# Performance work log

Measured on AMD Instinct MI355X. Metric: run time of the kernel, lower is better.

Reference implementation:

```python
import jax, jax.numpy as jnp
import numpy as np

FEATURE_DIM = 128

def setup_inputs() -> dict:
    key0 = jax.random.key(0)
    k1, k2, k3 = jax.random.split(key0, 3)
    B, NQ, NK, D = 4, 4096, 4096, FEATURE_DIM
    return {
        "target": jax.random.normal(k1, (B, NQ, D), dtype=jnp.float32),
        "key": jax.random.normal(k2, (B, NK, D), dtype=jnp.float32),
        "value": jax.random.normal(k3, (B, NK, D), dtype=jnp.float32),
    }

def reference(target, key, value):
    # Lan_K F: scores = target @ key^T / sqrt(d); weights = softmax(scores); out = weights @ value
    scale = 1.0 / np.sqrt(FEATURE_DIM).astype(np.float32)
    scores = jnp.einsum('bqd,bkd->bqk', target, key) * scale  # [B, NQ, NK]
    weights = jax.nn.softmax(scores, axis=-1)
    return jnp.einsum('bqk,bkd->bqd', weights, value)  # [B, NQ, D]
```

## Files before the change

kernel.cpp:

```cpp
#include <hip/hip_runtime.h>
#include <stdint.h>

#define B_ 4
#define NQ_ 4096
#define NK_ 4096
#define D_ 128
#define BM_ 32
#define BN_ 128
#define NITER_ (NK_/BN_)
#define PS_ 136
#define OS_ 66

typedef __attribute__((ext_vector_type(8))) short short8;
typedef __attribute__((ext_vector_type(4))) float floatx4;
typedef unsigned int u32;

union frag_u { u32 u[4]; short8 s; };
union pair_u { u32 u[2]; uint2 v; };

__device__ __forceinline__ unsigned short f2bf_rne(float x){
  union { float f; u32 u; } c; c.f = x;
  u32 u = c.u;
  return (unsigned short)((u + 0x7fffu + ((u >> 16) & 1u)) >> 16);
}
__device__ __forceinline__ u32 pk2bf(float a, float b){
  union { float f; u32 u; } x, y; x.f = a; y.f = b;
  return ((x.u + 0x8000u) >> 16) | ((y.u + 0x8000u) & 0xffff0000u);
}

__global__ __launch_bounds__(256) void prep_kernel(
    const float* __restrict__ k, const float* __restrict__ v,
    unsigned short* __restrict__ kf, unsigned short* __restrict__ vf){
  __shared__ __align__(16) char smem[40960];
  const int t = threadIdx.x;
  const int blk = blockIdx.x;
  if (blk < 128){
    int b = blk >> 5, it = blk & 31;
    const float* src = k + ((size_t)b*NK_ + it*BN_)*D_;
    #pragma unroll
    for (int i = 0; i < 16; i++){
      int f = t + i*256;
      int row = f >> 5, c4 = f & 31;
      float4 a = *(const float4*)(src + (size_t)row*D_ + c4*4);
      ushort4 s;
      s.x = f2bf_rne(a.x); s.y = f2bf_rne(a.y);
      s.z = f2bf_rne(a.z); s.w = f2bf_rne(a.w);
      int kg = row >> 5, rem = row & 31;
      int dh = (rem >> 2) & 1;
      int l15 = ((rem >> 3) << 2) | (rem & 3);
      int wq = kg*2 + dh;
      int j = c4 >> 3, l4 = (c4 >> 1) & 3, half = c4 & 1;
      *(ushort4*)(smem + (wq*4 + j)*1088 + l4*272 + l15*16 + half*8) = s;
    }
    __syncthreads();
    unsigned short* dst = kf + (size_t)(b*32 + it)*2048*8;
    #pragma unroll
    for (int i = 0; i < 8; i++){
      int c = t + i*256;
      int lane = c & 63, j = (c >> 6) & 3, wq = c >> 8;
      int l15 = lane & 15, l4 = lane >> 4;
      short8 x = *(const short8*)(smem + (wq*4 + j)*1088 + l4*272 + l15*16);
      *(short8*)(dst + (size_t)c*8) = x;
    }
  } else {
    int blk2 = blk - 128;
    int b = blk2 >> 5, it = blk2 & 31;
    const float* src = v + ((size_t)b*NK_ + it*BN_)*D_;
    #pragma unroll
    for (int i = 0; i < 16; i++){
      int f = t + i*256;
      int row = f >> 5, c4 = f & 31;
      float4 a = *(const float4*)(src + (size_t)row*D_ + c4*4);
      float vals[4] = {a.x, a.y, a.z, a.w};
      int kk = row & 7, l4a = (row >> 3) & 3, kga = row >> 5;
      #pragma unroll
      for (int jj = 0; jj < 4; jj++){
        int d = c4*4 + jj;
        int dh = d >> 6, dt = (d >> 4) & 3, l15 = d & 15;
        int c = ((kga*2 + dh)*4 + dt)*64 + l4a*16 + l15;
        *(unsigned short*)(smem + c*16 + (c>>2)*16 + kk*2) = f2bf_rne(vals[jj]);
      }
    }
    __syncthreads();
    unsigned short* dst = vf + (size_t)(b*32 + it)*2048*8;
    #pragma unroll
    for (int i = 0; i < 8; i++){
      int c = t + i*256;
      short8 x = *(const short8*)(smem + c*16 + (c>>2)*16);
      *(short8*)(dst + (size_t)c*8) = x;
    }
  }
}

__global__ __launch_bounds__(512, 4) void attn_kernel(
    const float* __restrict__ Qf, const unsigned short* __restrict__ Kb,
    const unsigned short* __restrict__ Vt, float* __restrict__ Out){
  __shared__ __align__(16) char sm[34816];
  unsigned short* smP = (unsigned short*)sm;
  float* smO = (float*)sm;
  float* smL = (float*)(sm + 33792);

  const int bi = blockIdx.x;
  const int b  = (bi >> 1) & 3;
  const int qt = ((bi >> 3) << 1) | (bi & 1);
  const int q0 = qt * BM_;
  const int tid = threadIdx.x;
  const int w = tid >> 6, lane = tid & 63;
  const int kg = w >> 1, dh = w & 1;
  const int l15 = lane & 15, l4 = lane >> 4;

  const short8* Kfrag = (const short8*)Kb;
  const short8* Vfrag = (const short8*)Vt;
  const size_t FSTRIDE = 8*4*64;
  const size_t fbase = ((size_t)b*256 + w)*256 + lane;

  short8 qf[2][4];
  {
    const float* qp = Qf + ((size_t)b*NQ_ + q0)*D_;
    #pragma unroll
    for (int nb = 0; nb < 2; nb++)
      #pragma unroll
      for (int kbq = 0; kbq < 4; kbq++){
        const float* p = qp + (size_t)(nb*16 + l15)*D_ + kbq*32 + l4*8;
        float4 a = *(const float4*)p;
        float4 c4 = *(const float4*)(p + 4);
        frag_u f;
        f.u[0] = pk2bf(a.x, a.y);  f.u[1] = pk2bf(a.z, a.w);
        f.u[2] = pk2bf(c4.x, c4.y); f.u[3] = pk2bf(c4.z, c4.w);
        qf[nb][kbq] = f.s;
      }
  }

  short8 kf[4], vf[4];
  #pragma unroll
  for (int j = 0; j < 4; j++) kf[j] = Kfrag[fbase + j*64];
  #pragma unroll
  for (int dt = 0; dt < 4; dt++) vf[dt] = Vfrag[fbase + dt*64];

  floatx4 o[2][4];
  #pragma unroll
  for (int nb = 0; nb < 2; nb++)
    #pragma unroll
    for (int dt = 0; dt < 4; dt++) o[nb][dt] = (floatx4)0.0f;
  float lsum[2] = {0.f, 0.f};

  const float SL = 0.08838834764831845f * 1.4426950408889634f;
  const size_t prow = (size_t)kg*32 + l4*8;

  for (int it = 0; it < NITER_; ++it){
    floatx4 s[2];
    #pragma unroll
    for (int nb = 0; nb < 2; nb++){
      s[nb] = (floatx4)0.0f;
      s[nb] = __builtin_amdgcn_mfma_f32_16x16x32_bf16(kf[0], qf[nb][0], s[nb], 0,0,0);
      s[nb] = __builtin_amdgcn_mfma_f32_16x16x32_bf16(kf[1], qf[nb][1], s[nb], 0,0,0);
      s[nb] = __builtin_amdgcn_mfma_f32_16x16x32_bf16(kf[2], qf[nb][2], s[nb], 0,0,0);
      s[nb] = __builtin_amdgcn_mfma_f32_16x16x32_bf16(kf[3], qf[nb][3], s[nb], 0,0,0);
    }
    if (it + 1 < NITER_){
      #pragma unroll
      for (int j = 0; j < 4; j++)
        kf[j] = Kfrag[fbase + (size_t)(it+1)*FSTRIDE + j*64];
    }
    unsigned short* smPb = smP + (it & 1) * (32 * PS_);
    #pragma unroll
    for (int nb = 0; nb < 2; nb++){
      float p0 = __builtin_amdgcn_exp2f(s[nb][0] * SL);
      float p1 = __builtin_amdgcn_exp2f(s[nb][1] * SL);
      float p2 = __builtin_amdgcn_exp2f(s[nb][2] * SL);
      float p3 = __builtin_amdgcn_exp2f(s[nb][3] * SL);
      lsum[nb] += (p0 + p1) + (p2 + p3);
      pair_u pp; pp.u[0] = pk2bf(p0, p1); pp.u[1] = pk2bf(p2, p3);
      *(uint2*)(smPb + (size_t)(nb*16 + l15)*PS_ + prow + dh*4) = pp.v;
    }
    asm volatile("s_waitcnt lgkmcnt(0)" ::: "memory");
    __builtin_amdgcn_s_barrier();
    asm volatile("" ::: "memory");
    #pragma unroll
    for (int nb = 0; nb < 2; nb++){
      short8 pf = *(const short8*)(smPb + (size_t)(nb*16 + l15)*PS_ + prow);
      o[nb][0] = __builtin_amdgcn_mfma_f32_16x16x32_bf16(pf, vf[0], o[nb][0], 0,0,0);
      o[nb][1] = __builtin_amdgcn_mfma_f32_16x16x32_bf16(pf, vf[1], o[nb][1], 0,0,0);
      o[nb][2] = __builtin_amdgcn_mfma_f32_16x16x32_bf16(pf, vf[2], o[nb][2], 0,0,0);
      o[nb][3] = __builtin_amdgcn_mfma_f32_16x16x32_bf16(pf, vf[3], o[nb][3], 0,0,0);
    }
    if (it + 1 < NITER_){
      #pragma unroll
      for (int dt = 0; dt < 4; dt++)
        vf[dt] = Vfrag[fbase + (size_t)(it+1)*FSTRIDE + dt*64];
    }
  }

  #pragma unroll
  for (int nb = 0; nb < 2; nb++){
    float v = lsum[nb];
    v += __shfl_xor(v, 16);
    v += __shfl_xor(v, 32);
    lsum[nb] = v;
  }
  if (l4 == 0)
    #pragma unroll
    for (int nb = 0; nb < 2; nb++)
      smL[w*32 + nb*16 + l15] = lsum[nb];

  __syncthreads();

  if (w >= 4){
    float* r = smO + (size_t)(w - 4) * 2112;
    #pragma unroll
    for (int nb = 0; nb < 2; nb++)
      #pragma unroll
      for (int dt = 0; dt < 4; dt++)
        #pragma unroll
        for (int q = 0; q < 4; q++)
          r[(size_t)(nb*16 + l4*4 + q)*OS_ + dt*16 + l15] = o[nb][dt][q];
  }
  __syncthreads();
  if (w < 4){
    float* r = smO + (size_t)w * 2112;
    #pragma unroll
    for (int nb = 0; nb < 2; nb++)
      #pragma unroll
      for (int dt = 0; dt < 4; dt++)
        #pragma unroll
        for (int q = 0; q < 4; q++)
          o[nb][dt][q] += r[(size_t)(nb*16 + l4*4 + q)*OS_ + dt*16 + l15];
  }
  __syncthreads();
  if (w == 2 || w == 3){
    float* r = smO + (size_t)(w - 2) * 2112;
    #pragma unroll
    for (int nb = 0; nb < 2; nb++)
      #pragma unroll
      for (int dt = 0; dt < 4; dt++)
        #pragma unroll
        for (int q = 0; q < 4; q++)
          r[(size_t)(nb*16 + l4*4 + q)*OS_ + dt*16 + l15] = o[nb][dt][q];
  }
  __syncthreads();
  if (w < 2){
    float* r = smO + (size_t)w * 2112;
    float* og = Out + ((size_t)b*NQ_ + q0)*D_ + dh*64;
    #pragma unroll
    for (int nb = 0; nb < 2; nb++)
      #pragma unroll
      for (int q = 0; q < 4; q++){
        int row = nb*16 + l4*4 + q;
        float lt = 0.f;
        #pragma unroll
        for (int w2 = 0; w2 < 8; w2++) lt += smL[w2*32 + row];
        float inv = 1.0f / lt;
        #pragma unroll
        for (int dt = 0; dt < 4; dt++){
          float val = o[nb][dt][q] + r[(size_t)row*OS_ + dt*16 + l15];
          og[(size_t)row*D_ + dt*16 + l15] = val * inv;
        }
      }
  }
}

extern "C" void kernel_launch(void* const* d_in, const int* in_sizes, int n_in,
                              void* d_out, int out_size, void* d_ws, size_t ws_size,
                              hipStream_t stream){
  const float* q = (const float*)d_in[0];
  const float* k = (const float*)d_in[1];
  const float* v = (const float*)d_in[2];
  float* out = (float*)d_out;
  unsigned short* kb = (unsigned short*)d_ws;
  unsigned short* vt = kb + (size_t)B_*NK_*D_;
  prep_kernel<<<256, 256, 0, stream>>>(k, v, kb, vt);
  attn_kernel<<<512, 512, 0, stream>>>(q, kb, vt, out);
}
```

Baseline: 123.0 us.

## Double query tile per block with 16 waves sharing K/V fragments

```diff
diff --git a/kernel.cpp b/kernel.cpp
--- a/kernel.cpp
+++ b/kernel.cpp
@@ -5,7 +5,7 @@
 #define NQ_ 4096
 #define NK_ 4096
 #define D_ 128
-#define BM_ 32
+#define BM_ 64
 #define BN_ 128
 #define NITER_ (NK_/BN_)
 #define PS_ 136
@@ -92,13 +92,13 @@
   }
 }
 
-__global__ __launch_bounds__(512, 4) void attn_kernel(
+__global__ __launch_bounds__(1024) void attn_kernel(
     const float* __restrict__ Qf, const unsigned short* __restrict__ Kb,
     const unsigned short* __restrict__ Vt, float* __restrict__ Out){
-  __shared__ __align__(16) char sm[34816];
+  __shared__ __align__(16) char sm[69632];
   unsigned short* smP = (unsigned short*)sm;
   float* smO = (float*)sm;
-  float* smL = (float*)(sm + 33792);
+  float* smL = (float*)(sm + 67584);
 
   const int bi = blockIdx.x;
   const int b  = (bi >> 1) & 3;
@@ -106,28 +106,31 @@
   const int q0 = qt * BM_;
   const int tid = threadIdx.x;
   const int w = tid >> 6, lane = tid & 63;
-  const int kg = w >> 1, dh = w & 1;
+  const int qh = w >> 3;
+  const int kg = (w >> 1) & 3;
+  const int dh = w & 1;
+  const int wq = w & 7;
   const int l15 = lane & 15, l4 = lane >> 4;
 
   const short8* Kfrag = (const short8*)Kb;
   const short8* Vfrag = (const short8*)Vt;
   const size_t FSTRIDE = 8*4*64;
-  const size_t fbase = ((size_t)b*256 + w)*256 + lane;
+  const size_t fbase = (((size_t)b*32)*8 + wq)*4*64 + lane;
 
   short8 qf[2][4];
   {
-    const float* qp = Qf + ((size_t)b*NQ_ + q0)*D_;
-    #pragma unroll
-    for (int nb = 0; nb < 2; nb++)
+    const float* qp = Qf + ((size_t)b*NQ_ + q0 + qh*32)*D_;
+    #pragma unroll
+    for (int n = 0; n < 2; n++)
       #pragma unroll
       for (int kbq = 0; kbq < 4; kbq++){
-        const float* p = qp + (size_t)(nb*16 + l15)*D_ + kbq*32 + l4*8;
+        const float* p = qp + (size_t)(n*16 + l15)*D_ + kbq*32 + l4*8;
         float4 a = *(const float4*)p;
         float4 c4 = *(const float4*)(p + 4);
         frag_u f;
         f.u[0] = pk2bf(a.x, a.y);  f.u[1] = pk2bf(a.z, a.w);
         f.u[2] = pk2bf(c4.x, c4.y); f.u[3] = pk2bf(c4.z, c4.w);
-        qf[nb][kbq] = f.s;
+        qf[n][kbq] = f.s;
       }
   }
 
@@ -139,9 +142,9 @@
 
   floatx4 o[2][4];
   #pragma unroll
-  for (int nb = 0; nb < 2; nb++)
-    #pragma unroll
-    for (int dt = 0; dt < 4; dt++) o[nb][dt] = (floatx4)0.0f;
+  for (int n = 0; n < 2; n++)
+    #pragma unroll
+    for (int dt = 0; dt < 4; dt++) o[n][dt] = (floatx4)0.0f;
   float lsum[2] = {0.f, 0.f};
 
   const float SL = 0.08838834764831845f * 1.4426950408889634f;
@@ -150,39 +153,39 @@
   for (int it = 0; it < NITER_; ++it){
     floatx4 s[2];
     #pragma unroll
-    for (int nb = 0; nb < 2; nb++){
-      s[nb] = (floatx4)0.0f;
-      s[nb] = __builtin_amdgcn_mfma_f32_16x16x32_bf16(kf[0], qf[nb][0], s[nb], 0,0,0);
-      s[nb] = __builtin_amdgcn_mfma_f32_16x16x32_bf16(kf[1], qf[nb][1], s[nb], 0,0,0);
-      s[nb] = __builtin_amdgcn_mfma_f32_16x16x32_bf16(kf[2], qf[nb][2], s[nb], 0,0,0);
-      s[nb] = __builtin_amdgcn_mfma_f32_16x16x32_bf16(kf[3], qf[nb][3], s[nb], 0,0,0);
+    for (int n = 0; n < 2; n++){
+      s[n] = (floatx4)0.0f;
+      s[n] = __builtin_amdgcn_mfma_f32_16x16x32_bf16(kf[0], qf[n][0], s[n], 0,0,0);
+      s[n] = __builtin_amdgcn_mfma_f32_16x16x32_bf16(kf[1], qf[n][1], s[n], 0,0,0);
+      s[n] = __builtin_amdgcn_mfma_f32_16x16x32_bf16(kf[2], qf[n][2], s[n], 0,0,0);
+      s[n] = __builtin_amdgcn_mfma_f32_16x16x32_bf16(kf[3], qf[n][3], s[n], 0,0,0);
     }
     if (it + 1 < NITER_){
       #pragma unroll
       for (int j = 0; j < 4; j++)
         kf[j] = Kfrag[fbase + (size_t)(it+1)*FSTRIDE + j*64];
     }
-    unsigned short* smPb = smP + (it & 1) * (32 * PS_);
-    #pragma unroll
-    for (int nb = 0; nb < 2; nb++){
-      float p0 = __builtin_amdgcn_exp2f(s[nb][0] * SL);
-      float p1 = __builtin_amdgcn_exp2f(s[nb][1] * SL);
-      float p2 = __builtin_amdgcn_exp2f(s[nb][2] * SL);
-      float p3 = __builtin_amdgcn_exp2f(s[nb][3] * SL);
-      lsum[nb] += (p0 + p1) + (p2 + p3);
+    unsigned short* smPb = smP + (it & 1) * (64 * PS_);
+    #pragma unroll
+    for (int n = 0; n < 2; n++){
+      float p0 = __builtin_amdgcn_exp2f(s[n][0] * SL);
+      float p1 = __builtin_amdgcn_exp2f(s[n][1] * SL);
+      float p2 = __builtin_amdgcn_exp2f(s[n][2] * SL);
+      float p3 = __builtin_amdgcn_exp2f(s[n][3] * SL);
+      lsum[n] += (p0 + p1) + (p2 + p3);
       pair_u pp; pp.u[0] = pk2bf(p0, p1); pp.u[1] = pk2bf(p2, p3);
-      *(uint2*)(smPb + (size_t)(nb*16 + l15)*PS_ + prow + dh*4) = pp.v;
+      *(uint2*)(smPb + (size_t)(qh*32 + n*16 + l15)*PS_ + prow + dh*4) = pp.v;
     }
     asm volatile("s_waitcnt lgkmcnt(0)" ::: "memory");
     __builtin_amdgcn_s_barrier();
     asm volatile("" ::: "memory");
     #pragma unroll
-    for (int nb = 0; nb < 2; nb++){
-      short8 pf = *(const short8*)(smPb + (size_t)(nb*16 + l15)*PS_ + prow);
-      o[nb][0] = __builtin_amdgcn_mfma_f32_16x16x32_bf16(pf, vf[0], o[nb][0], 0,0,0);
-      o[nb][1] = __builtin_amdgcn_mfma_f32_16x16x32_bf16(pf, vf[1], o[nb][1], 0,0,0);
-      o[nb][2] = __builtin_amdgcn_mfma_f32_16x16x32_bf16(pf, vf[2], o[nb][2], 0,0,0);
-      o[nb][3] = __builtin_amdgcn_mfma_f32_16x16x32_bf16(pf, vf[3], o[nb][3], 0,0,0);
+    for (int n = 0; n < 2; n++){
+      short8 pf = *(const short8*)(smPb + (size_t)(qh*32 + n*16 + l15)*PS_ + prow);
+      o[n][0] = __builtin_amdgcn_mfma_f32_16x16x32_bf16(pf, vf[0], o[n][0], 0,0,0);
+      o[n][1] = __builtin_amdgcn_mfma_f32_16x16x32_bf16(pf, vf[1], o[n][1], 0,0,0);
+      o[n][2] = __builtin_amdgcn_mfma_f32_16x16x32_bf16(pf, vf[2], o[n][2], 0,0,0);
+      o[n][3] = __builtin_amdgcn_mfma_f32_16x16x32_bf16(pf, vf[3], o[n][3], 0,0,0);
     }
     if (it + 1 < NITER_){
       #pragma unroll
@@ -192,68 +195,69 @@
   }
 
   #pragma unroll
-  for (int nb = 0; nb < 2; nb++){
-    float v = lsum[nb];
+  for (int n = 0; n < 2; n++){
+    float v = lsum[n];
     v += __shfl_xor(v, 16);
     v += __shfl_xor(v, 32);
-    lsum[nb] = v;
+    lsum[n] = v;
   }
   if (l4 == 0)
     #pragma unroll
-    for (int nb = 0; nb < 2; nb++)
-      smL[w*32 + nb*16 + l15] = lsum[nb];
-
-  __syncthreads();
-
-  if (w >= 4){
-    float* r = smO + (size_t)(w - 4) * 2112;
-    #pragma unroll
-    for (int nb = 0; nb < 2; nb++)
+    for (int n = 0; n < 2; n++)
+      smL[wq*64 + qh*32 + n*16 + l15] = lsum[n];
+
+  __syncthreads();
+
+  const int g = qh*2 + dh;
+  if (kg >= 2){
+    float* r = smO + (size_t)(g*2 + (kg-2)) * 2112;
+    #pragma unroll
+    for (int n = 0; n < 2; n++)
       #pragma unroll
       for (int dt = 0; dt < 4; dt++)
         #pragma unroll
         for (int q = 0; q < 4; q++)
-          r[(size_t)(nb*16 + l4*4 + q)*OS_ + dt*16 + l15] = o[nb][dt][q];
-  }
-  __syncthreads();
-  if (w < 4){
-    float* r = smO + (size_t)w * 2112;
-    #pragma unroll
-    for (int nb = 0; nb < 2; nb++)
+          r[(size_t)(n*16 + l4*4 + q)*OS_ + dt*16 + l15] = o[n][dt][q];
+  }
+  __syncthreads();
+  if (kg < 2){
+    float* r = smO + (size_t)(g*2 + kg) * 2112;
+    #pragma unroll
+    for (int n = 0; n < 2; n++)
       #pragma unroll
       for (int dt = 0; dt < 4; dt++)
         #pragma unroll
         for (int q = 0; q < 4; q++)
-          o[nb][dt][q] += r[(size_t)(nb*16 + l4*4 + q)*OS_ + dt*16 + l15];
-  }
-  __syncthreads();
-  if (w == 2 || w == 3){
-    float* r = smO + (size_t)(w - 2) * 2112;
-    #pragma unroll
-    for (int nb = 0; nb < 2; nb++)
+          o[n][dt][q] += r[(size_t)(n*16 + l4*4 + q)*OS_ + dt*16 + l15];
+  }
+  __syncthreads();
+  if (kg == 1){
+    float* r = smO + (size_t)g * 2112;
+    #pragma unroll
+    for (int n = 0; n < 2; n++)
       #pragma unroll
       for (int dt = 0; dt < 4; dt++)
         #pragma unroll
         for (int q = 0; q < 4; q++)
-          r[(size_t)(nb*16 + l4*4 + q)*OS_ + dt*16 + l15] = o[nb][dt][q];
-  }
-  __syncthreads();
-  if (w < 2){
-    float* r = smO + (size_t)w * 2112;
-    float* og = Out + ((size_t)b*NQ_ + q0)*D_ + dh*64;
-    #pragma unroll
-    for (int nb = 0; nb < 2; nb++)
+          r[(size_t)(n*16 + l4*4 + q)*OS_ + dt*16 + l15] = o[n][dt][q];
+  }
+  __syncthreads();
+  if (kg == 0){
+    float* r = smO + (size_t)g * 2112;
+    float* og = Out + ((size_t)b*NQ_ + q0 + qh*32)*D_ + dh*64;
+    #pragma unroll
+    for (int n = 0; n < 2; n++)
       #pragma unroll
       for (int q = 0; q < 4; q++){
-        int row = nb*16 + l4*4 + q;
+        int rowl = n*16 + l4*4 + q;
         float lt = 0.f;
         #pragma unroll
-        for (int w2 = 0; w2 < 8; w2++) lt += smL[w2*32 + row];
+        for (int w2 = 0; w2 < 8; w2++) lt += smL[w2*64 + qh*32 + rowl];
         float inv = 1.0f / lt;
         #pragma unroll
         for (int dt = 0; dt < 4; dt++){
-          float val = o[nb][dt][q] + r[(size_t)row*OS_ + dt*16 + l15];
-          og[(size_t)row*D_ + dt*16 + l15] = val * inv;
+          float val = o[n][dt][q] + r[(size_t)rowl*OS_ + dt*16 + l15];
+          og[(size_t)rowl*D_ + dt*16 + l15] = val * inv;
         }
       }
   }
@@ -269,5 +273,5 @@
   unsigned short* kb = (unsigned short*)d_ws;
   unsigned short* vt = kb + (size_t)B_*NK_*D_;
   prep_kernel<<<256, 256, 0, stream>>>(k, v, kb, vt);
-  attn_kernel<<<512, 512, 0, stream>>>(q, kb, vt, out);
-}
+  attn_kernel<<<256, 1024, 0, stream>>>(q, kb, vt, out);
+}
```

New measurement: 123.7 us. Within noise of the previous version (+0.5%).
